# Kernel optimization log

Hardware: AMD Instinct MI355X
Metric: run time of the kernel (lower is better)

## Reference

```python
import jax, jax.numpy as jnp
import numpy as np

HEADS = 4
HEAD_DIM = 32
WS = (8, 8)  # window size (h, w)


def _rel_bias_indices():
    idx = np.array([[i, j] for i in range(WS[0]) for j in range(WS[1])])  # [64,2]
    rel = idx[None, :, :] - idx[:, None, :]                               # [64,64,2]
    rel[:, :, 0] += WS[0] - 1
    rel[:, :, 1] += WS[1] - 1
    return rel

_REL = _rel_bias_indices()


def setup_inputs() -> dict:
    key = jax.random.key(0)
    ks = jax.random.split(key, 7)
    dim = 128
    inner = HEADS * HEAD_DIM
    return {
        "x": jax.random.normal(ks[0], (16, 128, 128, dim), dtype=jnp.float32),
        "w_qkv": jax.random.normal(ks[1], (dim, 3 * inner), dtype=jnp.float32) * 0.02,
        "w_out": jax.random.normal(ks[2], (inner, dim), dtype=jnp.float32) * 0.02,
        "b_out": jnp.zeros((dim,), dtype=jnp.float32),
        "pos_embedding": jax.random.normal(ks[3], (2 * WS[0] - 1, 2 * WS[1] - 1), dtype=jnp.float32) * 0.02,
        "ul_mask": jax.random.normal(ks[4], (WS[0] * WS[1], WS[0] * WS[1]), dtype=jnp.float32) * 0.02,
        "lr_mask": jax.random.normal(ks[5], (WS[0] * WS[1], WS[0] * WS[1]), dtype=jnp.float32) * 0.02,
    }


def _window_split(t, b, nw_h, nw_w):
    # (b, n_h, n_w, h*d) -> (b, h, nw, ws^2, d)
    t = t.reshape(b, nw_h, WS[0], nw_w, WS[1], HEADS, HEAD_DIM)
    t = t.transpose(0, 5, 1, 3, 2, 4, 6)
    return t.reshape(b, HEADS, nw_h * nw_w, WS[0] * WS[1], HEAD_DIM)


def reference(x, w_qkv, w_out, b_out, pos_embedding, ul_mask, lr_mask):
    b, n_h, n_w, _ = x.shape
    nw_h, nw_w = n_h // WS[0], n_w // WS[1]
    scale = HEAD_DIM ** -0.5
    disp = (WS[0] // 2, WS[1] // 2)

    # cyclic shift (torch.roll with shifts -ws//2)
    xs = jnp.roll(x, (-disp[0], -disp[1]), axis=(1, 2))

    qkv = xs @ w_qkv  # (b, n_h, n_w, 3*inner)
    q, k, v = jnp.split(qkv, 3, axis=-1)
    q = _window_split(q, b, nw_h, nw_w)
    k = _window_split(k, b, nw_h, nw_w)
    v = _window_split(v, b, nw_h, nw_w)

    dots = jnp.einsum('bhwid,bhwjd->bhwij', q, k) * scale
    bias = pos_embedding[_REL[:, :, 0], _REL[:, :, 1]]  # [64,64]
    dots = dots + bias
    # shift masks: bottom row of windows and last column of windows
    dots = dots.at[:, :, -nw_w:].add(ul_mask)
    dots = dots.at[:, :, nw_w - 1::nw_w].add(lr_mask)

    attn = jax.nn.softmax(dots, axis=-1)
    out = jnp.einsum('bhwij,bhwjd->bhwid', attn, v)

    # (b, h, nw, ws^2, d) -> (b, n_h, n_w, h*d)
    out = out.reshape(b, HEADS, nw_h, nw_w, WS[0], WS[1], HEAD_DIM)
    out = out.transpose(0, 2, 4, 3, 5, 1, 6).reshape(b, n_h, n_w, HEADS * HEAD_DIM)

    out = out @ w_out + b_out
    out = jnp.roll(out, (disp[0], disp[1]), axis=(1, 2))  # cyclic back shift
    return out
```

## Files before the change

### kernel.cpp

```cpp
#include <hip/hip_runtime.h>


typedef __bf16 bf16x8 __attribute__((ext_vector_type(8)));
typedef short  s16x8  __attribute__((ext_vector_type(8)));
typedef float  f32x4  __attribute__((ext_vector_type(4)));

static __device__ __forceinline__ float bf2f(unsigned short u) {
  unsigned x = ((unsigned)u) << 16;
  return __builtin_bit_cast(float, x);
}
static __device__ __forceinline__ unsigned short f2bf(float f) {
  unsigned x = __builtin_bit_cast(unsigned, f);
  x += 0x7FFFu + ((x >> 16) & 1u);
  return (unsigned short)(x >> 16);
}
static __device__ __forceinline__ f32x4 mfma16(s16x8 a, s16x8 b, f32x4 c) {
  return __builtin_amdgcn_mfma_f32_16x16x32_bf16(
      __builtin_bit_cast(bf16x8, a), __builtin_bit_cast(bf16x8, b), c, 0, 0, 0);
}

__global__ void prep_weights(const float* __restrict__ wqkv,
                             const float* __restrict__ wout,
                             unsigned short* __restrict__ wqkvT,
                             unsigned short* __restrict__ woutT) {
  int idx = blockIdx.x * blockDim.x + threadIdx.x;
  const int total1 = 384 * 128;
  if (idx < total1) {
    int n = idx >> 7, k = idx & 127;
    wqkvT[idx] = f2bf(wqkv[k * 384 + n]);
  } else {
    int i2 = idx - total1;
    int n = i2 >> 7, k = i2 & 127;
    woutT[i2] = f2bf(wout[k * 128 + n]);
  }
}

#define OFF_Q   0
#define OFF_K   17408
#define OFF_V   34816
#define OFF_S   53248
#define OFF_BO  90112
#define OFF_RS  107520
#define SMEM_SZ 108544

__global__ __launch_bounds__(1024, 4)
void swin_fused(const float* __restrict__ x,
                const unsigned short* __restrict__ wqkvT,
                const unsigned short* __restrict__ woutT,
                const float* __restrict__ b_out,
                const float* __restrict__ pe,
                const float* __restrict__ ulm,
                const float* __restrict__ lrm,
                float* __restrict__ out) {
  __shared__ __align__(16) unsigned char smem[SMEM_SZ];
  unsigned short* q_s  = (unsigned short*)(smem + OFF_Q);
  unsigned short* k_s  = (unsigned short*)(smem + OFF_K);
  unsigned short* v_s  = (unsigned short*)(smem + OFF_V);
  unsigned short* S_s  = (unsigned short*)(smem + OFF_S);
  unsigned short* xs_s = S_s;
  float*          bias_s = (float*)(smem + OFF_BO);
  unsigned short* oa_s   = (unsigned short*)(smem + OFF_BO);
  float*          rsum_s = (float*)(smem + OFF_RS);

  const int tid  = threadIdx.x;
  const int lane = tid & 63;
  const int wave = tid >> 6;
  const int ln15 = lane & 15;
  const int quad = lane >> 4;
  const int m_sub = quad << 2;

  const int bid = blockIdx.x;
  const int b   = bid >> 8;
  const int w   = bid & 255;
  const int wh  = w >> 4, ww = w & 15;

  {
    const int row0 = wh * 8, col0 = ww * 8;
#pragma unroll
    for (int it = 0; it < 2; ++it) {
      int t = tid + it * 1024;
      int tok = t >> 5, c4 = t & 31;
      int ti = tok >> 3, tj = tok & 7;
      int gi = (row0 + ti + 4) & 127;
      int gj = (col0 + tj + 4) & 127;
      float4 v4 = *(const float4*)(x + (((b * 128 + gi) * 128 + gj) * 128 + c4 * 4));
      ushort4 pk;
      pk.x = f2bf(v4.x); pk.y = f2bf(v4.y); pk.z = f2bf(v4.z); pk.w = f2bf(v4.w);
      *(ushort4*)(xs_s + tok * 136 + c4 * 4) = pk;
    }
    const bool has_ul = (wh == 15), has_lr = (ww == 15);
#pragma unroll
    for (int it = 0; it < 4; ++it) {
      int t = tid + it * 1024;
      int i = t >> 6, j = t & 63;
      int r0 = (j >> 3) - (i >> 3) + 7;
      int r1 = (j & 7) - (i & 7) + 7;
      float bsum = pe[r0 * 15 + r1];
      if (has_ul) bsum += ulm[t];
      if (has_lr) bsum += lrm[t];
      bias_s[i * 65 + j] = bsum;
    }
  }
  __syncthreads();

  {
    for (int nt = wave; nt < 24; nt += 16) {
      int n0 = nt * 16;
      int n  = n0 + ln15;
      s16x8 bfr[4];
      const unsigned short* wp = wqkvT + n * 128 + quad * 8;
#pragma unroll
      for (int ks = 0; ks < 4; ++ks) bfr[ks] = *(const s16x8*)(wp + ks * 32);
#pragma unroll
      for (int mt = 0; mt < 4; ++mt) {
        f32x4 acc = {0.f, 0.f, 0.f, 0.f};
#pragma unroll
        for (int ks = 0; ks < 4; ++ks) {
          s16x8 a = *(const s16x8*)(xs_s + (mt * 16 + ln15) * 136 + ks * 32 + quad * 8);
          acc = mfma16(a, bfr[ks], acc);
        }
        int tok0 = mt * 16 + m_sub;
        if (n0 < 128) {
#pragma unroll
          for (int r = 0; r < 4; ++r) q_s[(tok0 + r) * 136 + n] = f2bf(acc[r]);
        } else if (n0 < 256) {
          int nn = n - 128;
#pragma unroll
          for (int r = 0; r < 4; ++r) k_s[(tok0 + r) * 136 + nn] = f2bf(acc[r]);
        } else {
          int nn = n - 256;
          ushort4 pk;
          pk.x = f2bf(acc[0]); pk.y = f2bf(acc[1]);
          pk.z = f2bf(acc[2]); pk.w = f2bf(acc[3]);
          *(ushort4*)(v_s + nn * 72 + tok0) = pk;
        }
      }
    }
  }
  __syncthreads();

  {
    const int h  = wave >> 2;
    const int mt = wave & 3;
    unsigned short* Sh = S_s + h * 64 * 72;
    s16x8 qf = *(const s16x8*)(q_s + (mt * 16 + ln15) * 136 + h * 32 + quad * 8);
    const float scale = 0.17677669529663687f;
#pragma unroll
    for (int nt = 0; nt < 4; ++nt) {
      s16x8 kf = *(const s16x8*)(k_s + (nt * 16 + ln15) * 136 + h * 32 + quad * 8);
      f32x4 acc = {0.f, 0.f, 0.f, 0.f};
      acc = mfma16(qf, kf, acc);
      int nn = nt * 16 + ln15;
      int tok0 = mt * 16 + m_sub;
#pragma unroll
      for (int r = 0; r < 4; ++r) {
        float sv = acc[r] * scale + bias_s[(tok0 + r) * 65 + nn];
        Sh[(tok0 + r) * 72 + nn] = f2bf(sv);
      }
    }
  }
  __syncthreads();

  {
    const int h   = wave >> 2;
    const int row = (wave & 3) * 16 + ln15;
    unsigned short* rp = S_s + h * 64 * 72 + row * 72 + quad * 16;
    float vals[16];
    float mx = -1e30f;
#pragma unroll
    for (int c = 0; c < 2; ++c) {
      s16x8 s8 = *(const s16x8*)(rp + c * 8);
#pragma unroll
      for (int j = 0; j < 8; ++j) {
        float f = bf2f((unsigned short)s8[j]);
        vals[c * 8 + j] = f;
        mx = fmaxf(mx, f);
      }
    }
    mx = fmaxf(mx, __shfl_xor(mx, 16));
    mx = fmaxf(mx, __shfl_xor(mx, 32));
    float sum = 0.f;
#pragma unroll
    for (int c = 0; c < 2; ++c) {
      s16x8 st;
#pragma unroll
      for (int j = 0; j < 8; ++j) {
        float e = __expf(vals[c * 8 + j] - mx);
        sum += e;
        st[j] = (short)f2bf(e);
      }
      *(s16x8*)(rp + c * 8) = st;
    }
    sum += __shfl_xor(sum, 16);
    sum += __shfl_xor(sum, 32);
    if (quad == 0) rsum_s[h * 64 + row] = 1.0f / sum;
  }
  __syncthreads();

  {
    const int h  = wave >> 2;
    const int mt = wave & 3;
    unsigned short* Sh = S_s + h * 64 * 72;
    s16x8 pf[2];
#pragma unroll
    for (int ks = 0; ks < 2; ++ks)
      pf[ks] = *(const s16x8*)(Sh + (mt * 16 + ln15) * 72 + ks * 32 + quad * 8);
    int tok0 = mt * 16 + m_sub;
    float rc[4];
#pragma unroll
    for (int r = 0; r < 4; ++r) rc[r] = rsum_s[h * 64 + tok0 + r];
#pragma unroll
    for (int nt = 0; nt < 2; ++nt) {
      f32x4 acc = {0.f, 0.f, 0.f, 0.f};
#pragma unroll
      for (int ks = 0; ks < 2; ++ks) {
        s16x8 vf = *(const s16x8*)(v_s + (h * 32 + nt * 16 + ln15) * 72 + ks * 32 + quad * 8);
        acc = mfma16(pf[ks], vf, acc);
      }
      int n = h * 32 + nt * 16 + ln15;
#pragma unroll
      for (int r = 0; r < 4; ++r)
        oa_s[(tok0 + r) * 136 + n] = f2bf(acc[r] * rc[r]);
    }
  }
  __syncthreads();

  {
    const int nt  = wave >> 1;
    const int mtb = (wave & 1) * 2;
    int n = nt * 16 + ln15;
    s16x8 bfr[4];
    const unsigned short* wp = woutT + n * 128 + quad * 8;
#pragma unroll
    for (int ks = 0; ks < 4; ++ks) bfr[ks] = *(const s16x8*)(wp + ks * 32);
    float bo = b_out[n];
#pragma unroll
    for (int mi = 0; mi < 2; ++mi) {
      int mt = mtb + mi;
      f32x4 acc = {0.f, 0.f, 0.f, 0.f};
#pragma unroll
      for (int ks = 0; ks < 4; ++ks) {
        s16x8 a = *(const s16x8*)(oa_s + (mt * 16 + ln15) * 136 + ks * 32 + quad * 8);
        acc = mfma16(a, bfr[ks], acc);
      }
      int tok0 = mt * 16 + m_sub;
#pragma unroll
      for (int r = 0; r < 4; ++r) {
        int tok = tok0 + r;
        int ti = tok >> 3, tj = tok & 7;
        int gi = (wh * 8 + ti + 4) & 127;
        int gj = (ww * 8 + tj + 4) & 127;
        out[((b * 128 + gi) * 128 + gj) * 128 + n] = acc[r] + bo;
      }
    }
  }
}

extern "C" void kernel_launch(void* const* d_in, const int* in_sizes, int n_in,
                              void* d_out, int out_size, void* d_ws, size_t ws_size,
                              hipStream_t stream) {
  const float* x    = (const float*)d_in[0];
  const float* wqkv = (const float*)d_in[1];
  const float* wout = (const float*)d_in[2];
  const float* bout = (const float*)d_in[3];
  const float* pe   = (const float*)d_in[4];
  const float* ulm  = (const float*)d_in[5];
  const float* lrm  = (const float*)d_in[6];

  unsigned short* wqkvT = (unsigned short*)d_ws;
  unsigned short* woutT = wqkvT + 384 * 128;

  prep_weights<<<(384 * 128 + 128 * 128) / 256, 256, 0, stream>>>(wqkv, wout, wqkvT, woutT);
  swin_fused<<<16 * 256, 1024, 0, stream>>>(x, wqkvT, woutT, bout, pe, ulm, lrm,
                                            (float*)d_out);
}
```

Measured before the change: 350.5 us.

## Split fused Swin kernel into head-pair attention and separate projection kernels

The single 1024-thread-per-window kernel becomes two kernels. The first uses 256-thread blocks, one per window and head pair, to compute the QKV projection, attention and softmax in registers. It writes the bf16 attention output to a workspace. The second kernel reloads that output per window and applies the output projection with bias. The bias table (four mask variants) is also precomputed once in the prep kernel. The aim is smaller blocks with less shared memory, for more concurrent blocks per CU and fewer barriers. The cost is that each x tile is read and converted twice (once per head pair), plus an extra global round-trip for the intermediate activations.

```diff
diff --git a/kernel.cpp b/kernel.cpp
--- a/kernel.cpp
+++ b/kernel.cpp
@@ -5,10 +5,6 @@
 typedef short  s16x8  __attribute__((ext_vector_type(8)));
 typedef float  f32x4  __attribute__((ext_vector_type(4)));
 
-static __device__ __forceinline__ float bf2f(unsigned short u) {
-  unsigned x = ((unsigned)u) << 16;
-  return __builtin_bit_cast(float, x);
-}
 static __device__ __forceinline__ unsigned short f2bf(float f) {
   unsigned x = __builtin_bit_cast(unsigned, f);
   x += 0x7FFFu + ((x >> 16) & 1u);
@@ -19,48 +15,55 @@
       __builtin_bit_cast(bf16x8, a), __builtin_bit_cast(bf16x8, b), c, 0, 0, 0);
 }
 
-__global__ void prep_weights(const float* __restrict__ wqkv,
-                             const float* __restrict__ wout,
-                             unsigned short* __restrict__ wqkvT,
-                             unsigned short* __restrict__ woutT) {
-  int idx = blockIdx.x * blockDim.x + threadIdx.x;
-  const int total1 = 384 * 128;
-  if (idx < total1) {
+__global__ void prep(const float* __restrict__ wqkv,
+                     const float* __restrict__ wout,
+                     const float* __restrict__ pe,
+                     const float* __restrict__ ulm,
+                     const float* __restrict__ lrm,
+                     unsigned short* __restrict__ wqkvT,
+                     unsigned short* __restrict__ woutT,
+                     float* __restrict__ bias_g) {
+  int idx = blockIdx.x * 256 + threadIdx.x;
+  if (idx < 49152) {
     int n = idx >> 7, k = idx & 127;
     wqkvT[idx] = f2bf(wqkv[k * 384 + n]);
-  } else {
-    int i2 = idx - total1;
+  } else if (idx < 65536) {
+    int i2 = idx - 49152;
     int n = i2 >> 7, k = i2 & 127;
     woutT[i2] = f2bf(wout[k * 128 + n]);
-  }
-}
-
-#define OFF_Q   0
-#define OFF_K   17408
-#define OFF_V   34816
-#define OFF_S   53248
-#define OFF_BO  90112
-#define OFF_RS  107520
-#define SMEM_SZ 108544
-
-__global__ __launch_bounds__(1024, 4)
-void swin_fused(const float* __restrict__ x,
-                const unsigned short* __restrict__ wqkvT,
-                const unsigned short* __restrict__ woutT,
-                const float* __restrict__ b_out,
-                const float* __restrict__ pe,
-                const float* __restrict__ ulm,
-                const float* __restrict__ lrm,
-                float* __restrict__ out) {
-  __shared__ __align__(16) unsigned char smem[SMEM_SZ];
-  unsigned short* q_s  = (unsigned short*)(smem + OFF_Q);
-  unsigned short* k_s  = (unsigned short*)(smem + OFF_K);
-  unsigned short* v_s  = (unsigned short*)(smem + OFF_V);
-  unsigned short* S_s  = (unsigned short*)(smem + OFF_S);
-  unsigned short* xs_s = S_s;
-  float*          bias_s = (float*)(smem + OFF_BO);
-  unsigned short* oa_s   = (unsigned short*)(smem + OFF_BO);
-  float*          rsum_s = (float*)(smem + OFF_RS);
+  } else {
+    int i3 = idx - 65536;
+    int var = i3 >> 12, t = i3 & 4095;
+    int i = t >> 6, j = t & 63;
+    int r0 = (j >> 3) - (i >> 3) + 7;
+    int r1 = (j & 7) - (i & 7) + 7;
+    float v = pe[r0 * 15 + r1];
+    if (var & 2) v += ulm[t];
+    if (var & 1) v += lrm[t];
+    bias_g[i3] = v;
+  }
+}
+
+#define K1_OFF_P   0
+#define K1_OFF_Q   18432
+#define K1_OFF_K   27648
+#define K1_OFF_V   36864
+#define K1_OFF_RS  46080
+#define K1_SMEM    46592
+
+__global__ __launch_bounds__(256, 3)
+void swin_attn(const float* __restrict__ x,
+               const unsigned short* __restrict__ wqkvT,
+               const float* __restrict__ bias_g,
+               unsigned short* __restrict__ oa_ws) {
+  __shared__ __align__(16) unsigned char smem[K1_SMEM];
+  unsigned short* xs_s = (unsigned short*)(smem + K1_OFF_P);
+  unsigned short* P_s  = (unsigned short*)(smem + K1_OFF_P);
+  unsigned short* q_s  = (unsigned short*)(smem + K1_OFF_Q);
+  unsigned short* k_s  = (unsigned short*)(smem + K1_OFF_K);
+  unsigned short* oa_s = (unsigned short*)(smem + K1_OFF_Q);
+  unsigned short* v_s  = (unsigned short*)(smem + K1_OFF_V);
+  float*          rsum_s = (float*)(smem + K1_OFF_RS);
 
   const int tid  = threadIdx.x;
   const int lane = tid & 63;
@@ -70,15 +73,17 @@
   const int m_sub = quad << 2;
 
   const int bid = blockIdx.x;
-  const int b   = bid >> 8;
-  const int w   = bid & 255;
-  const int wh  = w >> 4, ww = w & 15;
+  const int b   = bid >> 9;
+  const int rem = bid & 511;
+  const int win = rem >> 1;
+  const int hp  = rem & 1;
+  const int wh  = win >> 4, ww = win & 15;
 
   {
     const int row0 = wh * 8, col0 = ww * 8;
 #pragma unroll
-    for (int it = 0; it < 2; ++it) {
-      int t = tid + it * 1024;
+    for (int it = 0; it < 8; ++it) {
+      int t = tid + it * 256;
       int tok = t >> 5, c4 = t & 31;
       int ti = tok >> 3, tj = tok & 7;
       int gi = (row0 + ti + 4) & 127;
@@ -88,27 +93,19 @@
       pk.x = f2bf(v4.x); pk.y = f2bf(v4.y); pk.z = f2bf(v4.z); pk.w = f2bf(v4.w);
       *(ushort4*)(xs_s + tok * 136 + c4 * 4) = pk;
     }
-    const bool has_ul = (wh == 15), has_lr = (ww == 15);
-#pragma unroll
-    for (int it = 0; it < 4; ++it) {
-      int t = tid + it * 1024;
-      int i = t >> 6, j = t & 63;
-      int r0 = (j >> 3) - (i >> 3) + 7;
-      int r1 = (j & 7) - (i & 7) + 7;
-      float bsum = pe[r0 * 15 + r1];
-      if (has_ul) bsum += ulm[t];
-      if (has_lr) bsum += lrm[t];
-      bias_s[i * 65 + j] = bsum;
-    }
-  }
-  __syncthreads();
-
-  {
-    for (int nt = wave; nt < 24; nt += 16) {
-      int n0 = nt * 16;
-      int n  = n0 + ln15;
+  }
+  __syncthreads();
+
+  {
+#pragma unroll
+    for (int i = 0; i < 3; ++i) {
+      int nt  = wave + 4 * i;
+      int sel = nt >> 2;
+      int ntl = nt & 3;
+      int nloc  = ntl * 16 + ln15;
+      int nglob = sel * 128 + hp * 64 + nloc;
       s16x8 bfr[4];
-      const unsigned short* wp = wqkvT + n * 128 + quad * 8;
+      const unsigned short* wp = wqkvT + nglob * 128 + quad * 8;
 #pragma unroll
       for (int ks = 0; ks < 4; ++ks) bfr[ks] = *(const s16x8*)(wp + ks * 32);
 #pragma unroll
@@ -120,19 +117,17 @@
           acc = mfma16(a, bfr[ks], acc);
         }
         int tok0 = mt * 16 + m_sub;
-        if (n0 < 128) {
-#pragma unroll
-          for (int r = 0; r < 4; ++r) q_s[(tok0 + r) * 136 + n] = f2bf(acc[r]);
-        } else if (n0 < 256) {
-          int nn = n - 128;
-#pragma unroll
-          for (int r = 0; r < 4; ++r) k_s[(tok0 + r) * 136 + nn] = f2bf(acc[r]);
+        if (sel == 0) {
+#pragma unroll
+          for (int r = 0; r < 4; ++r) q_s[(tok0 + r) * 72 + nloc] = f2bf(acc[r]);
+        } else if (sel == 1) {
+#pragma unroll
+          for (int r = 0; r < 4; ++r) k_s[(tok0 + r) * 72 + nloc] = f2bf(acc[r]);
         } else {
-          int nn = n - 256;
           ushort4 pk;
           pk.x = f2bf(acc[0]); pk.y = f2bf(acc[1]);
           pk.z = f2bf(acc[2]); pk.w = f2bf(acc[3]);
-          *(ushort4*)(v_s + nn * 72 + tok0) = pk;
+          *(ushort4*)(v_s + nloc * 72 + tok0) = pk;
         }
       }
     }
@@ -140,103 +135,139 @@
   __syncthreads();
 
   {
-    const int h  = wave >> 2;
-    const int mt = wave & 3;
-    unsigned short* Sh = S_s + h * 64 * 72;
-    s16x8 qf = *(const s16x8*)(q_s + (mt * 16 + ln15) * 136 + h * 32 + quad * 8);
+    const int hloc = wave >> 1;
+    const int mtb  = (wave & 1) * 2;
+    const int var  = ((wh == 15) ? 2 : 0) | ((ww == 15) ? 1 : 0);
+    const float* bg = bias_g + var * 4096;
     const float scale = 0.17677669529663687f;
 #pragma unroll
-    for (int nt = 0; nt < 4; ++nt) {
-      s16x8 kf = *(const s16x8*)(k_s + (nt * 16 + ln15) * 136 + h * 32 + quad * 8);
+    for (int mi = 0; mi < 2; ++mi) {
+      int mt = mtb + mi;
+      s16x8 qf = *(const s16x8*)(q_s + (mt * 16 + ln15) * 72 + hloc * 32 + quad * 8);
+      f32x4 acc[4];
+#pragma unroll
+      for (int nt = 0; nt < 4; ++nt) {
+        s16x8 kf = *(const s16x8*)(k_s + (nt * 16 + ln15) * 72 + hloc * 32 + quad * 8);
+        f32x4 z = {0.f, 0.f, 0.f, 0.f};
+        acc[nt] = mfma16(qf, kf, z);
+      }
+      float sc[4][4];
+#pragma unroll
+      for (int r = 0; r < 4; ++r) {
+        int row = mt * 16 + m_sub + r;
+#pragma unroll
+        for (int nt = 0; nt < 4; ++nt)
+          sc[r][nt] = acc[nt][r] * scale + bg[row * 64 + nt * 16 + ln15];
+      }
+      float sm[4];
+#pragma unroll
+      for (int r = 0; r < 4; ++r) {
+        float m0 = fmaxf(fmaxf(sc[r][0], sc[r][1]), fmaxf(sc[r][2], sc[r][3]));
+#pragma unroll
+        for (int d = 1; d < 16; d <<= 1) m0 = fmaxf(m0, __shfl_xor(m0, d));
+        float s0 = 0.f;
+#pragma unroll
+        for (int nt = 0; nt < 4; ++nt) {
+          float e = __expf(sc[r][nt] - m0);
+          sc[r][nt] = e;
+          s0 += e;
+        }
+#pragma unroll
+        for (int d = 1; d < 16; d <<= 1) s0 += __shfl_xor(s0, d);
+        sm[r] = s0;
+      }
+      unsigned short* Ph = P_s + hloc * 64 * 72;
+#pragma unroll
+      for (int r = 0; r < 4; ++r) {
+        int row = mt * 16 + m_sub + r;
+#pragma unroll
+        for (int nt = 0; nt < 4; ++nt)
+          Ph[row * 72 + nt * 16 + ln15] = f2bf(sc[r][nt]);
+        if (ln15 == 0) rsum_s[hloc * 64 + row] = 1.0f / sm[r];
+      }
+    }
+  }
+  __syncthreads();
+
+  {
+    const int hloc = wave >> 1;
+    const int ntv  = wave & 1;
+    const unsigned short* Ph = P_s + hloc * 64 * 72;
+    s16x8 vf[2];
+#pragma unroll
+    for (int ks = 0; ks < 2; ++ks)
+      vf[ks] = *(const s16x8*)(v_s + (hloc * 32 + ntv * 16 + ln15) * 72 + ks * 32 + quad * 8);
+#pragma unroll
+    for (int mt = 0; mt < 4; ++mt) {
       f32x4 acc = {0.f, 0.f, 0.f, 0.f};
-      acc = mfma16(qf, kf, acc);
-      int nn = nt * 16 + ln15;
+#pragma unroll
+      for (int ks = 0; ks < 2; ++ks) {
+        s16x8 pf = *(const s16x8*)(Ph + (mt * 16 + ln15) * 72 + ks * 32 + quad * 8);
+        acc = mfma16(pf, vf[ks], acc);
+      }
       int tok0 = mt * 16 + m_sub;
-#pragma unroll
-      for (int r = 0; r < 4; ++r) {
-        float sv = acc[r] * scale + bias_s[(tok0 + r) * 65 + nn];
-        Sh[(tok0 + r) * 72 + nn] = f2bf(sv);
-      }
-    }
-  }
-  __syncthreads();
-
-  {
-    const int h   = wave >> 2;
-    const int row = (wave & 3) * 16 + ln15;
-    unsigned short* rp = S_s + h * 64 * 72 + row * 72 + quad * 16;
-    float vals[16];
-    float mx = -1e30f;
-#pragma unroll
-    for (int c = 0; c < 2; ++c) {
-      s16x8 s8 = *(const s16x8*)(rp + c * 8);
-#pragma unroll
-      for (int j = 0; j < 8; ++j) {
-        float f = bf2f((unsigned short)s8[j]);
-        vals[c * 8 + j] = f;
-        mx = fmaxf(mx, f);
-      }
-    }
-    mx = fmaxf(mx, __shfl_xor(mx, 16));
-    mx = fmaxf(mx, __shfl_xor(mx, 32));
-    float sum = 0.f;
-#pragma unroll
-    for (int c = 0; c < 2; ++c) {
-      s16x8 st;
-#pragma unroll
-      for (int j = 0; j < 8; ++j) {
-        float e = __expf(vals[c * 8 + j] - mx);
-        sum += e;
-        st[j] = (short)f2bf(e);
-      }
-      *(s16x8*)(rp + c * 8) = st;
-    }
-    sum += __shfl_xor(sum, 16);
-    sum += __shfl_xor(sum, 32);
-    if (quad == 0) rsum_s[h * 64 + row] = 1.0f / sum;
-  }
-  __syncthreads();
-
-  {
-    const int h  = wave >> 2;
-    const int mt = wave & 3;
-    unsigned short* Sh = S_s + h * 64 * 72;
-    s16x8 pf[2];
-#pragma unroll
-    for (int ks = 0; ks < 2; ++ks)
-      pf[ks] = *(const s16x8*)(Sh + (mt * 16 + ln15) * 72 + ks * 32 + quad * 8);
-    int tok0 = mt * 16 + m_sub;
-    float rc[4];
-#pragma unroll
-    for (int r = 0; r < 4; ++r) rc[r] = rsum_s[h * 64 + tok0 + r];
-#pragma unroll
-    for (int nt = 0; nt < 2; ++nt) {
-      f32x4 acc = {0.f, 0.f, 0.f, 0.f};
-#pragma unroll
-      for (int ks = 0; ks < 2; ++ks) {
-        s16x8 vf = *(const s16x8*)(v_s + (h * 32 + nt * 16 + ln15) * 72 + ks * 32 + quad * 8);
-        acc = mfma16(pf[ks], vf, acc);
-      }
-      int n = h * 32 + nt * 16 + ln15;
+      int cloc = hloc * 32 + ntv * 16 + ln15;
 #pragma unroll
       for (int r = 0; r < 4; ++r)
-        oa_s[(tok0 + r) * 136 + n] = f2bf(acc[r] * rc[r]);
-    }
-  }
-  __syncthreads();
-
-  {
-    const int nt  = wave >> 1;
-    const int mtb = (wave & 1) * 2;
-    int n = nt * 16 + ln15;
+        oa_s[(tok0 + r) * 72 + cloc] = f2bf(acc[r] * rsum_s[hloc * 64 + tok0 + r]);
+    }
+  }
+  __syncthreads();
+
+  {
+    unsigned short* dst = oa_ws + (((size_t)b * 512 + win * 2 + hp) * 64) * 64;
+#pragma unroll
+    for (int it = 0; it < 2; ++it) {
+      int idx = tid + it * 256;
+      int row = idx >> 3, c = idx & 7;
+      *(s16x8*)(dst + row * 64 + c * 8) = *(const s16x8*)(oa_s + row * 72 + c * 8);
+    }
+  }
+}
+
+__global__ __launch_bounds__(256, 4)
+void swin_proj(const unsigned short* __restrict__ oa_ws,
+               const unsigned short* __restrict__ woutT,
+               const float* __restrict__ b_out,
+               float* __restrict__ out) {
+  __shared__ __align__(16) unsigned short oa_s[64 * 136];
+
+  const int tid  = threadIdx.x;
+  const int lane = tid & 63;
+  const int wave = tid >> 6;
+  const int ln15 = lane & 15;
+  const int quad = lane >> 4;
+  const int m_sub = quad << 2;
+
+  const int bid = blockIdx.x;
+  const int b   = bid >> 8;
+  const int win = bid & 255;
+  const int wh  = win >> 4, ww = win & 15;
+
+  {
+    const unsigned short* src = oa_ws + (((size_t)b * 512 + win * 2) * 64) * 64;
+#pragma unroll
+    for (int it = 0; it < 4; ++it) {
+      int idx = tid + it * 256;
+      int hp  = idx >> 9;
+      int tok = (idx >> 3) & 63;
+      int c   = idx & 7;
+      *(s16x8*)(oa_s + tok * 136 + hp * 64 + c * 8) =
+          *(const s16x8*)(src + ((size_t)hp * 64 + tok) * 64 + c * 8);
+    }
+  }
+  __syncthreads();
+
+#pragma unroll
+  for (int ni = 0; ni < 2; ++ni) {
+    int n = (wave * 2 + ni) * 16 + ln15;
     s16x8 bfr[4];
     const unsigned short* wp = woutT + n * 128 + quad * 8;
 #pragma unroll
     for (int ks = 0; ks < 4; ++ks) bfr[ks] = *(const s16x8*)(wp + ks * 32);
     float bo = b_out[n];
 #pragma unroll
-    for (int mi = 0; mi < 2; ++mi) {
-      int mt = mtb + mi;
+    for (int mt = 0; mt < 4; ++mt) {
       f32x4 acc = {0.f, 0.f, 0.f, 0.f};
 #pragma unroll
       for (int ks = 0; ks < 4; ++ks) {
@@ -268,9 +299,11 @@
   const float* lrm  = (const float*)d_in[6];
 
   unsigned short* wqkvT = (unsigned short*)d_ws;
-  unsigned short* woutT = wqkvT + 384 * 128;
-
-  prep_weights<<<(384 * 128 + 128 * 128) / 256, 256, 0, stream>>>(wqkv, wout, wqkvT, woutT);
-  swin_fused<<<16 * 256, 1024, 0, stream>>>(x, wqkvT, woutT, bout, pe, ulm, lrm,
-                                            (float*)d_out);
-}
+  unsigned short* woutT = wqkvT + 49152;
+  float*          bias_g = (float*)(woutT + 16384);
+  unsigned short* oa_ws  = (unsigned short*)(bias_g + 16384);
+
+  prep<<<320, 256, 0, stream>>>(wqkv, wout, pe, ulm, lrm, wqkvT, woutT, bias_g);
+  swin_attn<<<16 * 256 * 2, 256, 0, stream>>>(x, wqkvT, bias_g, oa_ws);
+  swin_proj<<<16 * 256, 256, 0, stream>>>(oa_ws, woutT, bout, (float*)d_out);
+}
```

Result: slower. 365.5 us (+4.3%).
